# Optimization experiments

Hardware: AMD Instinct MI355X
Metric: run time of the kernel (lower is better)

Reference implementation:

```python
import jax, jax.numpy as jnp
import numpy as np


def setup_inputs() -> dict:
    key = jax.random.key(0)
    k1, k2, k3, k4 = jax.random.split(key, 4)
    T, H, I, E, K = 4096, 1024, 1024, 8, 2
    hidden_states = jax.random.normal(k1, (T, H), dtype=jnp.float32)
    router_logits = jax.random.normal(k2, (T, E), dtype=jnp.float32)
    # fused gate+up projection: [E, H, 2*I]; down projection: [E, I, H]
    up_weight = jax.random.normal(k3, (E, H, 2 * I), dtype=jnp.float32) * 0.02
    down_weight = jax.random.normal(k4, (E, I, H), dtype=jnp.float32) * 0.02
    return {"hidden_states": hidden_states, "router_logits": router_logits,
            "up_weight": up_weight, "down_weight": down_weight, "topk": K}


def reference(hidden_states, router_logits, up_weight, down_weight, topk):
    T, H = hidden_states.shape
    E = up_weight.shape[0]
    I = down_weight.shape[1]
    K = topk
    # select_experts: softmax over all experts, top-k, renormalize weights
    probs = jax.nn.softmax(router_logits, axis=-1)
    topk_w, topk_ids = jax.lax.top_k(probs, K)               # [T, K]
    topk_w = topk_w / jnp.sum(topk_w, axis=-1, keepdims=True)
    # expand tokens: each token is dispatched K times (grouped-GEMM operand)
    xk = jnp.repeat(hidden_states, K, axis=0)                # [T*K, H]
    flat_ids = topk_ids.reshape(-1)                          # [T*K]
    acc = jnp.zeros((T * K, H), dtype=hidden_states.dtype)
    for e in range(E):  # fixed small expert loop (grouped GEMM semantics)
        mask = (flat_ids == e).astype(hidden_states.dtype)[:, None]
        xe = xk * mask                                       # zero out non-e tokens
        gu = xe @ up_weight[e]                               # [T*K, 2I]
        h = jax.nn.silu(gu[:, :I]) * gu[:, I:]               # gated SiLU
        acc = acc + h @ down_weight[e]                       # [T*K, H]
    # combine: weighted sum over the K expert slots (reduce step)
    out = jnp.einsum('tk,tkh->th', topk_w, acc.reshape(T, K, H))
    return out
```

## Files before the change

kernel.cpp:

```cpp
#include <hip/hip_runtime.h>
#include <hip/hip_bf16.h>


#define T_TOK 4096
#define HDIM  1024
#define NEXP  8
#define RROWS (T_TOK * 2)
#define MAXPE T_TOK

typedef unsigned short u16;
typedef short v8s __attribute__((ext_vector_type(8)));
typedef float v4f __attribute__((ext_vector_type(4)));
typedef __attribute__((address_space(3))) unsigned int as3_u32;
typedef const __attribute__((address_space(1))) unsigned int as1_u32c;

__device__ __forceinline__ float b2f(u16 u) {
    union { unsigned int i; float f; } v; v.i = ((unsigned int)u) << 16; return v.f;
}
__device__ __forceinline__ u16 f2b(float f) {
    union { float f; unsigned int i; } v; v.f = f;
    unsigned int x = v.i;
    return (u16)((x + 0x7FFFu + ((x >> 16) & 1u)) >> 16);
}
__device__ __forceinline__ unsigned int pack2(float a, float b) {
    return (unsigned int)f2b(a) | ((unsigned int)f2b(b) << 16);
}
__device__ __forceinline__ void stage16(const u16* g, u16* l) {
    __builtin_amdgcn_global_load_lds((as1_u32c*)g, (as3_u32*)l, 16, 0, 0);
}

__device__ __forceinline__ void cvt_tile(const float* __restrict__ Wb,
                                         u16* __restrict__ Wtb,
                                         int N, int n0b, int k0b, u16* sm) {
    const int tid = threadIdx.x;
    const int m = tid & 15, rr = tid >> 4;
    float4 f[16];
#pragma unroll
    for (int s = 0; s < 4; s++)
#pragma unroll
        for (int j = 0; j < 4; j++)
            f[s * 4 + j] = *(const float4*)(Wb + (size_t)(k0b + s * 64 + rr * 4 + j) * N
                                               + n0b + m * 4);
#pragma unroll
    for (int s = 0; s < 4; s++) {
        const int kc = s * 16 + rr;
        const float* fp = (const float*)&f[s * 4];
#pragma unroll
        for (int nl = 0; nl < 4; nl++) {
            int n_l = m * 4 + nl;
            uint2 v;
            v.x = pack2(fp[nl], fp[4 + nl]);
            v.y = pack2(fp[8 + nl], fp[12 + nl]);
            *(uint2*)&sm[n_l * 256 + ((kc ^ (n_l & 15)) << 2)] = v;
        }
    }
    __syncthreads();
    const int n_l = tid >> 2, q = tid & 3, sw = n_l & 15;
    u16* dst = Wtb + (size_t)(n0b + n_l) * 1024 + k0b + q * 64;
#pragma unroll
    for (int c2 = 0; c2 < 8; c2++) {
        uint2 a = *(const uint2*)&sm[n_l * 256 + (((q * 16 + 2 * c2) ^ sw) << 2)];
        uint2 b = *(const uint2*)&sm[n_l * 256 + (((q * 16 + 2 * c2 + 1) ^ sw) << 2)];
        uint4 o; o.x = a.x; o.y = a.y; o.z = b.x; o.w = b.y;
        *(uint4*)(dst + c2 * 8) = o;
    }
}

__global__ __launch_bounds__(256)
void prep_all(const float* __restrict__ X, const float* __restrict__ RL,
              const float* __restrict__ WU,
              u16* __restrict__ Xb, u16* __restrict__ WtU,
              int* __restrict__ ids, float* __restrict__ wts,
              int* __restrict__ counts, int* __restrict__ rowbuf) {
    __shared__ __align__(16) u16 sm[64 * 256];
    const int bx = blockIdx.x;
    const int tid = threadIdx.x;

    if (bx < 1024) {
        int e = bx >> 7, r = bx & 127;
        int nt = r >> 2, kt = r & 3;
        cvt_tile(WU + (size_t)e * 1024 * 2048, WtU + (size_t)e * 2048 * 1024,
                 2048, nt * 64, kt * 256, sm);
    } else if (bx < 1536) {
        int base = (bx - 1024) * 8192 + tid * 4;
#pragma unroll
        for (int j = 0; j < 8; j++) {
            float4 fx = *(const float4*)(X + base + j * 1024);
            uint2 o; o.x = pack2(fx.x, fx.y); o.y = pack2(fx.z, fx.w);
            *(uint2*)(Xb + base + j * 1024) = o;
        }
    } else {
        int t = (bx - 1536) * 256 + tid;
        float4 a = *(const float4*)(RL + t * NEXP);
        float4 b = *(const float4*)(RL + t * NEXP + 4);
        float l[NEXP] = {a.x, a.y, a.z, a.w, b.x, b.y, b.z, b.w};
        int i0 = 0;
#pragma unroll
        for (int q = 1; q < NEXP; q++) if (l[q] > l[i0]) i0 = q;
        int i1 = (i0 == 0) ? 1 : 0;
#pragma unroll
        for (int q = 0; q < NEXP; q++) if (q != i0 && l[q] > l[i1]) i1 = q;
        float w0 = 1.0f / (1.0f + expf(l[i1] - l[i0]));
        ids[2 * t] = i0;     ids[2 * t + 1] = i1;
        wts[2 * t] = w0;     wts[2 * t + 1] = 1.0f - w0;
        int p0 = atomicAdd(&counts[i0], 1);
        rowbuf[i0 * MAXPE + p0] = 2 * t;
        int p1 = atomicAdd(&counts[i1], 1);
        rowbuf[i1 * MAXPE + p1] = 2 * t + 1;
    }
}

template<int PHASE>
__global__ __launch_bounds__(256)
void mfma_gemm(const u16* __restrict__ A, const u16* __restrict__ Bt,
               u16* __restrict__ H,
               const int* __restrict__ counts, const int* __restrict__ rowbuf,
               const float* __restrict__ WD, u16* __restrict__ WtD,
               const float* __restrict__ wts, float* __restrict__ out) {
    __shared__ __align__(16) u16 smem[4 * 128 * 64];
    __shared__ int srid[128];
    const int bi0 = blockIdx.x;

    int bi;
    if (PHASE == 1) {
        if ((bi0 % 9) == 8) {
            int ci = bi0 / 9;
            int e = ci >> 6, r = ci & 63;
            int nt = r >> 2, kt = r & 3;
            cvt_tile(WD + (size_t)e * 1024 * 1024, WtD + (size_t)e * 1024 * 1024,
                     1024, nt * 64, kt * 256, smem);
            return;
        }
        bi = (bi0 / 9) * 8 + (bi0 % 9);
    } else {
        bi = bi0;
    }

    const int xcd = bi & 7, kb = bi >> 3;
    int e, ct, rt;
    if (PHASE == 1) { int p = (kb & 15) * 8 + xcd; e = p >> 4; ct = p & 15; rt = kb >> 4; }
    else            { int p = (kb & 7) * 8 + xcd;  e = p >> 3; ct = p & 7;  rt = kb >> 3; }
    const int cnt = counts[e];
    if (rt * 128 >= cnt) return;
    const int tid = threadIdx.x;
    const int lane = tid & 63, wave = tid >> 6;

    u16* sA0 = smem;
    u16* sB0 = smem + 8192;
    u16* sA1 = smem + 16384;
    u16* sB1 = smem + 24576;

    if (tid < 128) {
        int idx = rt * 128 + tid;
        srid[tid] = (idx < cnt) ? rowbuf[e * MAXPE + idx] : -1;
    }
    __syncthreads();

    const int lrow = lane >> 3;
    const int lchunk = (lane & 7) ^ lrow;
    const u16* aPtr[4]; const u16* bPtr[4];
    int offs[4];
#pragma unroll
    for (int p = 0; p < 4; p++) {
        int region = p * 4 + wave;
        int r = region * 8 + lrow;
        int rid = srid[r];
        int arow = (rid < 0) ? 0 : (PHASE == 1 ? (rid >> 1) : rid);
        aPtr[p] = A + (size_t)arow * 1024 + lchunk * 8;
        int n;
        if (PHASE == 1) n = (r < 64) ? (ct * 64 + r) : (1024 + ct * 64 + (r - 64));
        else            n = ct * 128 + r;
        bPtr[p] = Bt + (size_t)e * (PHASE == 1 ? 2048 : 1024) * 1024
                     + (size_t)n * 1024 + lchunk * 8;
        offs[p] = region * 512 + lane * 8;
    }

    const int quad = lane >> 4, mr = lane & 15;
    const int swA = mr & 7;
    const v4f zf = {0.f, 0.f, 0.f, 0.f};
    v4f acc[2][8];
#pragma unroll
    for (int i = 0; i < 2; i++)
#pragma unroll
        for (int j = 0; j < 8; j++) acc[i][j] = zf;

    auto stageAll = [&](u16* sAx, u16* sBx, int kk) {
#pragma unroll
        for (int p = 0; p < 4; p++) {
            stage16(aPtr[p] + kk * 64, sAx + offs[p]);
            stage16(bPtr[p] + kk * 64, sBx + offs[p]);
        }
    };
    auto computeTile = [&](const u16* sAx, const u16* sBx) {
#pragma unroll
        for (int kh = 0; kh < 2; kh++) {
            const int c = kh * 4 + quad;
            v8s a0 = *(const v8s*)(sAx + (wave * 32 + mr) * 64 + ((c ^ swA) * 8));
            v8s a1 = *(const v8s*)(sAx + (wave * 32 + 16 + mr) * 64 + ((c ^ swA) * 8));
#pragma unroll
            for (int nf = 0; nf < 8; nf++) {
                v8s b = *(const v8s*)(sBx + (nf * 16 + mr) * 64 + ((c ^ swA) * 8));
                acc[0][nf] = __builtin_amdgcn_mfma_f32_16x16x32_bf16(a0, b, acc[0][nf], 0, 0, 0);
                acc[1][nf] = __builtin_amdgcn_mfma_f32_16x16x32_bf16(a1, b, acc[1][nf], 0, 0, 0);
            }
        }
    };

    stageAll(sA0, sB0, 0);
    __syncthreads();
#pragma unroll 1
    for (int kt = 0; kt < 8; kt++) {
        stageAll(sA1, sB1, 2 * kt + 1);
        computeTile(sA0, sB0);
        __syncthreads();
        if (kt < 7) stageAll(sA0, sB0, 2 * kt + 2);
        computeTile(sA1, sB1);
        __syncthreads();
    }

#pragma unroll
    for (int mf = 0; mf < 2; mf++) {
#pragma unroll
        for (int reg = 0; reg < 4; reg++) {
            int rl = wave * 32 + mf * 16 + quad * 4 + reg;
            int grow = srid[rl];
            if (grow < 0) continue;
            if (PHASE == 1) {
                size_t base = (size_t)grow * 1024 + ct * 64 + mr;
#pragma unroll
                for (int nf = 0; nf < 4; nf++) {
                    float g = acc[mf][nf][reg], u = acc[mf][nf + 4][reg];
                    H[base + nf * 16] = f2b((g / (1.0f + expf(-g))) * u);
                }
            } else {
                float w = wts[grow];
                float* ob = out + (size_t)(grow >> 1) * 1024 + ct * 128 + mr;
#pragma unroll
                for (int nf = 0; nf < 8; nf++)
                    atomicAdd(ob + nf * 16, w * acc[mf][nf][reg]);
            }
        }
    }
}

__global__ void combine_kernel(const u16* __restrict__ accb,
                               const float* __restrict__ wts,
                               float* __restrict__ out) {
    int g = blockIdx.x * blockDim.x + threadIdx.x;
    int t = g >> 8;
    int c = (g & 255) * 4;
    float w0 = wts[2 * t], w1 = wts[2 * t + 1];
    ushort4 a = *(const ushort4*)(accb + (size_t)(2 * t) * 1024 + c);
    ushort4 b = *(const ushort4*)(accb + (size_t)(2 * t + 1) * 1024 + c);
    float4 o;
    o.x = w0 * b2f(a.x) + w1 * b2f(b.x);
    o.y = w0 * b2f(a.y) + w1 * b2f(b.y);
    o.z = w0 * b2f(a.z) + w1 * b2f(b.z);
    o.w = w0 * b2f(a.w) + w1 * b2f(b.w);
    *(float4*)(out + (size_t)t * 1024 + c) = o;
}

__global__ void router_kernel(const float* __restrict__ logits,
                              int* __restrict__ ids, float* __restrict__ wts) {
    int t = blockIdx.x * blockDim.x + threadIdx.x;
    if (t >= T_TOK) return;
    float4 a = *(const float4*)(logits + t * NEXP);
    float4 b = *(const float4*)(logits + t * NEXP + 4);
    float l[NEXP] = {a.x, a.y, a.z, a.w, b.x, b.y, b.z, b.w};
    int i0 = 0;
#pragma unroll
    for (int i = 1; i < NEXP; i++) if (l[i] > l[i0]) i0 = i;
    int i1 = (i0 == 0) ? 1 : 0;
#pragma unroll
    for (int i = 0; i < NEXP; i++) if (i != i0 && l[i] > l[i1]) i1 = i;
    float w0 = 1.0f / (1.0f + expf(l[i1] - l[i0]));
    ids[2 * t] = i0;     ids[2 * t + 1] = i1;
    wts[2 * t] = w0;     wts[2 * t + 1] = 1.0f - w0;
}

__global__ void bucket_kernel(const int* __restrict__ ids,
                              int* __restrict__ counts, int* __restrict__ rowbuf) {
    int r = blockIdx.x * blockDim.x + threadIdx.x;
    if (r >= RROWS) return;
    int e = ids[r];
    int pos = atomicAdd(&counts[e], 1);
    rowbuf[e * MAXPE + pos] = r;
}

template<int GATED, int AF32>
__global__ __launch_bounds__(256)
void moe_gemm_kernel(const void* __restrict__ Av,
                     const float* __restrict__ B,
                     u16* __restrict__ C,
                     const int* __restrict__ counts,
                     const int* __restrict__ rowbuf,
                     int rowShift, int NB) {
    const int e   = blockIdx.z;
    const int cnt = counts[e];
    const int rt  = blockIdx.y;
    if (rt * 128 >= cnt) return;
    const int ct  = blockIdx.x;
    const int tid = threadIdx.x;

    __shared__ __align__(16) u16 sA[128 * 40];
    __shared__ __align__(16) u16 sB[(GATED ? 2 : 1) * 64 * 40];
    __shared__ int srid[128];

    if (tid < 128) {
        int idx = rt * 128 + tid;
        srid[tid] = (idx < cnt) ? rowbuf[e * MAXPE + idx] : -1;
    }
    __syncthreads();

    const int ar = tid >> 1, ac = (tid & 1) * 16;
    int arid = srid[ar];
    const float* aSrcF = 0; const u16* aSrcH = 0;
    if (arid >= 0) {
        if (AF32) aSrcF = (const float*)Av + (size_t)(arid >> rowShift) * HDIM + ac;
        else      aSrcH = (const u16*)Av + (size_t)(arid >> rowShift) * HDIM + ac;
    }
    u16* aDst = sA + ar * 40 + ac;

    const int kq2 = (tid >> 4) * 2, n4 = (tid & 15) * 4;
    const float* bSrcG = B + (size_t)e * 1024 * NB + (size_t)kq2 * NB + ct * 64 + n4;
    const float* bSrcU = bSrcG + 1024;

    const int lane = tid & 63, wave = tid >> 6;
    const int quad = lane >> 4, mr = lane & 15;

    const v4f zf = {0.f, 0.f, 0.f, 0.f};
    v4f accG[2][4], accU[2][4];
#pragma unroll
    for (int i = 0; i < 2; i++)
#pragma unroll
        for (int j = 0; j < 4; j++) { accG[i][j] = zf; accU[i][j] = zf; }

    for (int kk = 0; kk < HDIM / 32; kk++) {
        uint4 aw0 = make_uint4(0, 0, 0, 0), aw1 = make_uint4(0, 0, 0, 0);
        if (AF32) {
            if (aSrcF) {
                float4 f0 = *(const float4*)(aSrcF + kk * 32);
                float4 f1 = *(const float4*)(aSrcF + kk * 32 + 4);
                float4 f2 = *(const float4*)(aSrcF + kk * 32 + 8);
                float4 f3 = *(const float4*)(aSrcF + kk * 32 + 12);
                aw0 = make_uint4(pack2(f0.x, f0.y), pack2(f0.z, f0.w),
                                 pack2(f1.x, f1.y), pack2(f1.z, f1.w));
                aw1 = make_uint4(pack2(f2.x, f2.y), pack2(f2.z, f2.w),
                                 pack2(f3.x, f3.y), pack2(f3.z, f3.w));
            }
        } else {
            if (aSrcH) {
                aw0 = *(const uint4*)(aSrcH + kk * 32);
                aw1 = *(const uint4*)(aSrcH + kk * 32 + 8);
            }
        }
        const size_t bOff = (size_t)kk * 32 * NB;
        float4 g0 = *(const float4*)(bSrcG + bOff);
        float4 g1 = *(const float4*)(bSrcG + bOff + NB);
        float4 u0 = make_float4(0, 0, 0, 0), u1 = make_float4(0, 0, 0, 0);
        if (GATED) {
            u0 = *(const float4*)(bSrcU + bOff);
            u1 = *(const float4*)(bSrcU + bOff + NB);
        }

        __syncthreads();
        *(uint4*)aDst = aw0;
        *(uint4*)(aDst + 8) = aw1;
        {
            const float gx[4] = {g0.x, g0.y, g0.z, g0.w};
            const float gy[4] = {g1.x, g1.y, g1.z, g1.w};
#pragma unroll
            for (int j = 0; j < 4; j++)
                *(unsigned int*)&sB[(n4 + j) * 40 + kq2] = pack2(gx[j], gy[j]);
            if (GATED) {
                const float ux[4] = {u0.x, u0.y, u0.z, u0.w};
                const float uy[4] = {u1.x, u1.y, u1.z, u1.w};
#pragma unroll
                for (int j = 0; j < 4; j++)
                    *(unsigned int*)&sB[64 * 40 + (n4 + j) * 40 + kq2] = pack2(ux[j], uy[j]);
            }
        }
        __syncthreads();

        v8s af0 = *(const v8s*)(sA + (wave * 32 + mr) * 40 + quad * 8);
        v8s af1 = *(const v8s*)(sA + (wave * 32 + 16 + mr) * 40 + quad * 8);
#pragma unroll
        for (int nf = 0; nf < 4; nf++) {
            v8s bg = *(const v8s*)(sB + (nf * 16 + mr) * 40 + quad * 8);
            accG[0][nf] = __builtin_amdgcn_mfma_f32_16x16x32_bf16(af0, bg, accG[0][nf], 0, 0, 0);
            accG[1][nf] = __builtin_amdgcn_mfma_f32_16x16x32_bf16(af1, bg, accG[1][nf], 0, 0, 0);
            if (GATED) {
                v8s bu = *(const v8s*)(sB + 64 * 40 + (nf * 16 + mr) * 40 + quad * 8);
                accU[0][nf] = __builtin_amdgcn_mfma_f32_16x16x32_bf16(af0, bu, accU[0][nf], 0, 0, 0);
                accU[1][nf] = __builtin_amdgcn_mfma_f32_16x16x32_bf16(af1, bu, accU[1][nf], 0, 0, 0);
            }
        }
    }

#pragma unroll
    for (int mf = 0; mf < 2; mf++) {
#pragma unroll
        for (int reg = 0; reg < 4; reg++) {
            int rl = wave * 32 + mf * 16 + quad * 4 + reg;
            int grow = srid[rl];
            if (grow < 0) continue;
            size_t base = (size_t)grow * 1024 + ct * 64 + mr;
#pragma unroll
            for (int nf = 0; nf < 4; nf++) {
                float g = accG[mf][nf][reg];
                float val;
                if (GATED) {
                    float u = accU[mf][nf][reg];
                    val = (g / (1.0f + expf(-g))) * u;
                } else {
                    val = g;
                }
                C[base + nf * 16] = f2b(val);
            }
        }
    }
}

extern "C" void kernel_launch(void* const* d_in, const int* in_sizes, int n_in,
                              void* d_out, int out_size, void* d_ws, size_t ws_size,
                              hipStream_t stream) {
    const float *X = 0, *RL = 0, *WU = 0, *WD = 0;
    for (int i = 0; i < n_in; i++) {
        switch (in_sizes[i]) {
            case T_TOK * HDIM:        X  = (const float*)d_in[i]; break;
            case T_TOK * NEXP:        RL = (const float*)d_in[i]; break;
            case NEXP * HDIM * 2048:  WU = (const float*)d_in[i]; break;
            case NEXP * HDIM * 1024:  WD = (const float*)d_in[i]; break;
            default: break;
        }
    }
    if (!X)  X  = (const float*)d_in[0];
    if (!RL) RL = (const float*)d_in[1];
    if (!WU) WU = (const float*)d_in[2];
    if (!WD) WD = (const float*)d_in[3];
    float* OUT = (float*)d_out;

    char* ws = (char*)d_ws;
    int*   ids    = (int*)(ws + 0);
    float* wts    = (float*)(ws + 32768);
    int*   counts = (int*)(ws + 65536);
    int*   rowbuf = (int*)(ws + 65792);
    u16* Xb   = (u16*)(ws + 196864);
    u16* WtU  = (u16*)(ws + 8585472);
    u16* WtD  = (u16*)(ws + 42139904);
    u16* HbufF= (u16*)(ws + 58917120);
    const size_t needFast = 75694336ull;
    u16* Hbuf = (u16*)(ws + 196864);
    u16* Acc  = (u16*)(ws + 196864 + 16777216);

    hipMemsetAsync(counts, 0, NEXP * sizeof(int), stream);

    if (ws_size >= needFast) {
        hipMemsetAsync(OUT, 0, (size_t)T_TOK * HDIM * sizeof(float), stream);
        prep_all<<<1552, 256, 0, stream>>>(
            X, RL, WU, Xb, WtU, ids, wts, counts, rowbuf);
        mfma_gemm<1><<<4608, 256, 0, stream>>>(Xb, WtU, HbufF, counts, rowbuf,
                                               WD, WtD, (const float*)0, (float*)0);
        mfma_gemm<2><<<2048, 256, 0, stream>>>(HbufF, WtD, (u16*)0, counts, rowbuf,
                                               (const float*)0, (u16*)0, wts, OUT);
    } else {
        router_kernel<<<T_TOK / 256, 256, 0, stream>>>(RL, ids, wts);
        bucket_kernel<<<RROWS / 256, 256, 0, stream>>>(ids, counts, rowbuf);
        moe_gemm_kernel<1, 1><<<dim3(16, 32, NEXP), 256, 0, stream>>>(
            (const void*)X, WU, Hbuf, counts, rowbuf, 1, 2048);
        moe_gemm_kernel<0, 0><<<dim3(16, 32, NEXP), 256, 0, stream>>>(
            (const void*)Hbuf, WD, Acc, counts, rowbuf, 0, 1024);
        combine_kernel<<<T_TOK, 256, 0, stream>>>(Acc, wts, OUT);
    }
}
```

Before: 300.1 us.

## Move down-weight conversion to prep, replace atomic combine, relax k-loop barriers

Moves the down-projection weight bf16 transpose out of the phase-1 GEMM grid and into the prep kernel. Phase 2 now writes per-slot bf16 results into a buffer that reuses the up-weight region, and a separate combine kernel applies the routing weights, replacing the fp32 atomicAdds and the output memset. The GEMM k-loop swaps __syncthreads for raw s_barrier with partial vmcnt waits so that global loads can stay in flight across barriers. The trade-offs are an extra kernel launch, an extra bf16 round trip on the accumulator, and a dependence on the assumed in-flight load count for correctness.

Result: faster. 278.5 us (-7.2%).

```diff
diff --git a/kernel.cpp b/kernel.cpp
--- a/kernel.cpp
+++ b/kernel.cpp
@@ -68,8 +68,8 @@
 
 __global__ __launch_bounds__(256)
 void prep_all(const float* __restrict__ X, const float* __restrict__ RL,
-              const float* __restrict__ WU,
-              u16* __restrict__ Xb, u16* __restrict__ WtU,
+              const float* __restrict__ WU, const float* __restrict__ WD,
+              u16* __restrict__ Xb, u16* __restrict__ WtU, u16* __restrict__ WtD,
               int* __restrict__ ids, float* __restrict__ wts,
               int* __restrict__ counts, int* __restrict__ rowbuf) {
     __shared__ __align__(16) u16 sm[64 * 256];
@@ -89,7 +89,7 @@
             uint2 o; o.x = pack2(fx.x, fx.y); o.y = pack2(fx.z, fx.w);
             *(uint2*)(Xb + base + j * 1024) = o;
         }
-    } else {
+    } else if (bx < 1552) {
         int t = (bx - 1536) * 256 + tid;
         float4 a = *(const float4*)(RL + t * NEXP);
         float4 b = *(const float4*)(RL + t * NEXP + 4);
@@ -107,6 +107,12 @@
         rowbuf[i0 * MAXPE + p0] = 2 * t;
         int p1 = atomicAdd(&counts[i1], 1);
         rowbuf[i1 * MAXPE + p1] = 2 * t + 1;
+    } else {
+        int ci = bx - 1552;
+        int e = ci >> 6, r = ci & 63;
+        int nt = r >> 2, kt = r & 3;
+        cvt_tile(WD + (size_t)e * 1024 * 1024, WtD + (size_t)e * 1024 * 1024,
+                 1024, nt * 64, kt * 256, sm);
     }
 }
 
@@ -114,28 +120,10 @@
 __global__ __launch_bounds__(256)
 void mfma_gemm(const u16* __restrict__ A, const u16* __restrict__ Bt,
                u16* __restrict__ H,
-               const int* __restrict__ counts, const int* __restrict__ rowbuf,
-               const float* __restrict__ WD, u16* __restrict__ WtD,
-               const float* __restrict__ wts, float* __restrict__ out) {
+               const int* __restrict__ counts, const int* __restrict__ rowbuf) {
     __shared__ __align__(16) u16 smem[4 * 128 * 64];
     __shared__ int srid[128];
-    const int bi0 = blockIdx.x;
-
-    int bi;
-    if (PHASE == 1) {
-        if ((bi0 % 9) == 8) {
-            int ci = bi0 / 9;
-            int e = ci >> 6, r = ci & 63;
-            int nt = r >> 2, kt = r & 3;
-            cvt_tile(WD + (size_t)e * 1024 * 1024, WtD + (size_t)e * 1024 * 1024,
-                     1024, nt * 64, kt * 256, smem);
-            return;
-        }
-        bi = (bi0 / 9) * 8 + (bi0 % 9);
-    } else {
-        bi = bi0;
-    }
-
+    const int bi = blockIdx.x;
     const int xcd = bi & 7, kb = bi >> 3;
     int e, ct, rt;
     if (PHASE == 1) { int p = (kb & 15) * 8 + xcd; e = p >> 4; ct = p & 15; rt = kb >> 4; }
@@ -207,15 +195,22 @@
     };
 
     stageAll(sA0, sB0, 0);
-    __syncthreads();
 #pragma unroll 1
     for (int kt = 0; kt < 8; kt++) {
         stageAll(sA1, sB1, 2 * kt + 1);
+        asm volatile("s_waitcnt vmcnt(8)" ::: "memory");
+        __builtin_amdgcn_s_barrier();
         computeTile(sA0, sB0);
-        __syncthreads();
-        if (kt < 7) stageAll(sA0, sB0, 2 * kt + 2);
+        __builtin_amdgcn_s_barrier();
+        if (kt < 7) {
+            stageAll(sA0, sB0, 2 * kt + 2);
+            asm volatile("s_waitcnt vmcnt(8)" ::: "memory");
+        } else {
+            asm volatile("s_waitcnt vmcnt(0)" ::: "memory");
+        }
+        __builtin_amdgcn_s_barrier();
         computeTile(sA1, sB1);
-        __syncthreads();
+        __builtin_amdgcn_s_barrier();
     }
 
 #pragma unroll
@@ -233,11 +228,10 @@
                     H[base + nf * 16] = f2b((g / (1.0f + expf(-g))) * u);
                 }
             } else {
-                float w = wts[grow];
-                float* ob = out + (size_t)(grow >> 1) * 1024 + ct * 128 + mr;
+                size_t base = (size_t)grow * 1024 + ct * 128 + mr;
 #pragma unroll
                 for (int nf = 0; nf < 8; nf++)
-                    atomicAdd(ob + nf * 16, w * acc[mf][nf][reg]);
+                    H[base + nf * 16] = f2b(acc[mf][nf][reg]);
             }
         }
     }
@@ -449,6 +443,7 @@
     u16* WtU  = (u16*)(ws + 8585472);
     u16* WtD  = (u16*)(ws + 42139904);
     u16* HbufF= (u16*)(ws + 58917120);
+    u16* AccF = WtU;
     const size_t needFast = 75694336ull;
     u16* Hbuf = (u16*)(ws + 196864);
     u16* Acc  = (u16*)(ws + 196864 + 16777216);
@@ -456,13 +451,11 @@
     hipMemsetAsync(counts, 0, NEXP * sizeof(int), stream);
 
     if (ws_size >= needFast) {
-        hipMemsetAsync(OUT, 0, (size_t)T_TOK * HDIM * sizeof(float), stream);
-        prep_all<<<1552, 256, 0, stream>>>(
-            X, RL, WU, Xb, WtU, ids, wts, counts, rowbuf);
-        mfma_gemm<1><<<4608, 256, 0, stream>>>(Xb, WtU, HbufF, counts, rowbuf,
-                                               WD, WtD, (const float*)0, (float*)0);
-        mfma_gemm<2><<<2048, 256, 0, stream>>>(HbufF, WtD, (u16*)0, counts, rowbuf,
-                                               (const float*)0, (u16*)0, wts, OUT);
+        prep_all<<<2064, 256, 0, stream>>>(
+            X, RL, WU, WD, Xb, WtU, WtD, ids, wts, counts, rowbuf);
+        mfma_gemm<1><<<4096, 256, 0, stream>>>(Xb, WtU, HbufF, counts, rowbuf);
+        mfma_gemm<2><<<2048, 256, 0, stream>>>(HbufF, WtD, AccF, counts, rowbuf);
+        combine_kernel<<<T_TOK, 256, 0, stream>>>(AccF, wts, OUT);
     } else {
         router_kernel<<<T_TOK / 256, 256, 0, stream>>>(RL, ids, wts);
         bucket_kernel<<<RROWS / 256, 256, 0, stream>>>(ids, counts, rowbuf);
```
